# Kernel tuning notes

Measured on AMD Instinct MI355X. Metric: run time of the kernel, lower is better.

## Reference

```python
import jax, jax.numpy as jnp
import numpy as np

N = 50000      # nodes
E = 1_000_000  # edges (avg degree 20)
D = 64         # hidden dim
L = 3          # num dynamics layers
LN_EPS = 1e-5


def layernorm(h, g, b):
    mu = jnp.mean(h, axis=-1, keepdims=True)
    var = jnp.mean(jnp.square(h - mu), axis=-1, keepdims=True)
    return (h - mu) * jax.lax.rsqrt(var + LN_EPS) * g + b


def transformer_conv(h, src, dst, Wq, bq, Wk, bk, Wv, bv, Ws, bs):
    # PyG TransformerConv, heads=1, concat=False, beta=False, root_weight=True
    n = h.shape[0]
    d = Wq.shape[1]
    q = h @ Wq + bq            # [N, D] queries (dst side)
    k = h @ Wk + bk            # [N, D] keys   (src side)
    v = h @ Wv + bv            # [N, D] values (src side)
    logits = jnp.sum(q[dst] * k[src], axis=-1) / jnp.sqrt(jnp.asarray(d, h.dtype))  # [E]
    # segment softmax over incoming edges of each dst node
    m = jax.ops.segment_max(logits, dst, num_segments=n)      # [N]
    e = jnp.exp(logits - m[dst])                               # [E]
    s = jax.ops.segment_sum(e, dst, num_segments=n)            # [N]
    a = e / s[dst]                                             # [E]
    agg = jax.ops.segment_sum(a[:, None] * v[src], dst, num_segments=n)  # [N, D]
    return agg + h @ Ws + bs   # root/skip connection


def setup_inputs() -> dict:
    key = jax.random.key(0)
    ks = jax.random.split(key, 24)
    w = lambda k, shape: (jax.random.normal(k, shape, jnp.float32) * 0.05)
    inp = {
        "x": jax.random.normal(ks[0], (N, D), jnp.float32),
        "edge_index": jax.random.randint(ks[1], (2, E), 0, N, jnp.int32),
        # input_proj conv params
        "Wq0": w(ks[2], (D, D)), "bq0": w(ks[3], (D,)),
        "Wk0": w(ks[4], (D, D)), "bk0": w(ks[5], (D,)),
        "Wv0": w(ks[6], (D, D)), "bv0": w(ks[7], (D,)),
        "Ws0": w(ks[8], (D, D)), "bs0": w(ks[9], (D,)),
        "ln0_g": jnp.ones((D,), jnp.float32), "ln0_b": jnp.zeros((D,), jnp.float32),
        # stacked dynamics conv params [L, ...]
        "Wq": w(ks[10], (L, D, D)), "bq": w(ks[11], (L, D)),
        "Wk": w(ks[12], (L, D, D)), "bk": w(ks[13], (L, D)),
        "Wv": w(ks[14], (L, D, D)), "bv": w(ks[15], (L, D)),
        "Ws": w(ks[16], (L, D, D)), "bs": w(ks[17], (L, D)),
        "ln_g": jnp.ones((L, D), jnp.float32), "ln_b": jnp.zeros((L, D), jnp.float32),
    }
    return inp


def reference(x, edge_index, Wq0, bq0, Wk0, bk0, Wv0, bv0, Ws0, bs0, ln0_g, ln0_b,
              Wq, bq, Wk, bk, Wv, bv, Ws, bs, ln_g, ln_b):
    src, dst = edge_index[0], edge_index[1]
    h = transformer_conv(x, src, dst, Wq0, bq0, Wk0, bk0, Wv0, bv0, Ws0, bs0)
    h = jax.nn.relu(layernorm(h, ln0_g, ln0_b))
    # dropout is identity in eval mode
    for i in range(L):
        hi = transformer_conv(h, src, dst, Wq[i], bq[i], Wk[i], bk[i],
                              Wv[i], bv[i], Ws[i], bs[i])
        h = jax.nn.relu(layernorm(hi + h, ln_g[i], ln_b[i]))
    return h
```

## Files before the change

kernel.cpp:

```cpp
#include <hip/hip_runtime.h>
#include <math.h>


#define DD 64

typedef __attribute__((ext_vector_type(8))) _Float16 h8;
typedef __attribute__((ext_vector_type(2))) _Float16 h2;
typedef __attribute__((ext_vector_type(4))) float f32x4;

__device__ __forceinline__ unsigned short f2h(float f) {
    union { _Float16 h; unsigned short u; } c;
    c.h = (_Float16)f;
    return c.u;
}
__device__ __forceinline__ h2 u2h2(unsigned u) {
    union { unsigned u; h2 h; } c; c.u = u; return c.h;
}
__device__ __forceinline__ unsigned pk2u(float a, float b) {
    union { decltype(__builtin_amdgcn_cvt_pkrtz(0.f, 0.f)) h; unsigned u; } c;
    c.h = __builtin_amdgcn_cvt_pkrtz(a, b);
    return c.u;
}
__device__ __forceinline__ float h2dot(h2 a, h2 b, float c) {
#if __has_builtin(__builtin_amdgcn_fdot2)
    return __builtin_amdgcn_fdot2(a, b, c, false);
#else
    return fmaf((float)a[0], (float)b[0], fmaf((float)a[1], (float)b[1], c));
#endif
}

__global__ void count_rank(const int* __restrict__ dst, int* __restrict__ counts,
                           int* __restrict__ rank, int E) {
    int e = blockIdx.x * blockDim.x + threadIdx.x;
    if (e < E) rank[e] = atomicAdd(&counts[dst[e]], 1);
}

__global__ __launch_bounds__(1024) void scan_local(const int* __restrict__ counts,
                                                   int* __restrict__ localscan,
                                                   int* __restrict__ blockSums, int n) {
    __shared__ int sh[1024];
    int i = blockIdx.x * 1024 + threadIdx.x;
    int val = (i < n) ? counts[i] : 0;
    sh[threadIdx.x] = val;
    __syncthreads();
    for (int off = 1; off < 1024; off <<= 1) {
        int t = (threadIdx.x >= off) ? sh[threadIdx.x - off] : 0;
        __syncthreads();
        sh[threadIdx.x] += t;
        __syncthreads();
    }
    if (i < n) localscan[i] = sh[threadIdx.x] - val;
    if (threadIdx.x == 1023) blockSums[blockIdx.x] = sh[1023];
}

__global__ __launch_bounds__(64) void scan_tops(int* __restrict__ blockSums, int nb) {
    int i = threadIdx.x;
    int val = (i < nb) ? blockSums[i] : 0;
    int s = val;
#pragma unroll
    for (int off = 1; off < 64; off <<= 1) {
        int t = __shfl_up(s, off, 64);
        if (i >= off) s += t;
    }
    if (i < nb) blockSums[i] = s - val;
}

__global__ void emit_rowptr(const int* __restrict__ localscan,
                            const int* __restrict__ blockSums,
                            int* __restrict__ row_ptr, int n, int E) {
    int i = blockIdx.x * blockDim.x + threadIdx.x;
    if (i < n) row_ptr[i] = localscan[i] + blockSums[i >> 10];
    if (i == 0) row_ptr[n] = E;
}

__global__ void scatter_edges(const int* __restrict__ src, const int* __restrict__ dst,
                              const int* __restrict__ rank, const int* __restrict__ row_ptr,
                              int* __restrict__ col, int E) {
    int e = blockIdx.x * blockDim.x + threadIdx.x;
    if (e < E) col[row_ptr[dst[e]] + rank[e]] = src[e] << 8;
}

__global__ void prep_all(const float* __restrict__ x, unsigned short* __restrict__ hbf,
                         int nD,
                         const float* __restrict__ W0, const float* __restrict__ W1,
                         const float* __restrict__ W2, const float* __restrict__ W3,
                         const float* __restrict__ Wqs, const float* __restrict__ Wks,
                         const float* __restrict__ Wvs, const float* __restrict__ Wss,
                         unsigned short* __restrict__ Wt) {
    int i = blockIdx.x * blockDim.x + threadIdx.x;
    if (i < nD) { hbf[i] = f2h(x[i]); return; }
    int id = i - nD;
    if (id >= 16 * 4096) return;
    int mat = id >> 12, rem = id & 4095;
    int nn = rem >> 6, kk = rem & 63;
    int layer = mat >> 2, wh = mat & 3;
    const float* W;
    if (layer == 0) W = wh == 0 ? W0 : wh == 1 ? W1 : wh == 2 ? W2 : W3;
    else {
        const float* base = wh == 0 ? Wqs : wh == 1 ? Wks : wh == 2 ? Wvs : Wss;
        W = base + (size_t)(layer - 1) * 4096;
    }
    float val = W[kk * 64 + nn];
    if (wh == 0) val *= 0.125f;
    Wt[id] = f2h(val);
}

__global__ __launch_bounds__(256) void gemm_mfma(
    const unsigned short* __restrict__ hbf, const unsigned short* __restrict__ Wt,
    const float* __restrict__ Bq, const float* __restrict__ Bk,
    const float* __restrict__ Bv, const float* __restrict__ Bs,
    const float* __restrict__ hprev,
    unsigned short* __restrict__ qO, unsigned short* __restrict__ kvO,
    float* __restrict__ sO, int ntiles) {
    int lane = threadIdx.x & 63;
    int wave = threadIdx.x >> 6;
    int ml = lane & 15, ql = lane >> 4;

    const unsigned short* W = Wt + wave * 4096;
    h8 wfrag[4][2];
#pragma unroll
    for (int t = 0; t < 4; ++t)
#pragma unroll
        for (int kh = 0; kh < 2; ++kh)
            wfrag[t][kh] = *(const h8*)(W + (t * 16 + ml) * 64 + kh * 32 + ql * 8);

    const float* bias = wave == 0 ? Bq : wave == 1 ? Bk : wave == 2 ? Bv : Bs;
    float4 bias4[4];
#pragma unroll
    for (int t = 0; t < 4; ++t) {
        bias4[t] = *(const float4*)(bias + t * 16 + ql * 4);
        if (wave == 0) {
            bias4[t].x *= 0.125f; bias4[t].y *= 0.125f;
            bias4[t].z *= 0.125f; bias4[t].w *= 0.125f;
        }
    }

    for (int tile = blockIdx.x; tile < ntiles; tile += gridDim.x) {
        int node0 = tile * 16;
        h8 hfrag[2];
#pragma unroll
        for (int kh = 0; kh < 2; ++kh)
            hfrag[kh] = *(const h8*)(hbf + (size_t)(node0 + ml) * 64 + kh * 32 + ql * 8);
        f32x4 acc[4];
#pragma unroll
        for (int t = 0; t < 4; ++t) {
            acc[t][0] = bias4[t].x; acc[t][1] = bias4[t].y;
            acc[t][2] = bias4[t].z; acc[t][3] = bias4[t].w;
        }
#pragma unroll
        for (int t = 0; t < 4; ++t)
#pragma unroll
            for (int kh = 0; kh < 2; ++kh)
                acc[t] = __builtin_amdgcn_mfma_f32_16x16x32_f16(
                    wfrag[t][kh], hfrag[kh], acc[t], 0, 0, 0);

        size_t rowe = (size_t)(node0 + ml) * 64;
        if (wave == 0) {
#pragma unroll
            for (int t = 0; t < 4; ++t) {
                uint2 st;
                st.x = pk2u(acc[t][0], acc[t][1]);
                st.y = pk2u(acc[t][2], acc[t][3]);
                *(uint2*)(qO + rowe + t * 16 + ql * 4) = st;
            }
        } else if (wave == 3) {
#pragma unroll
            for (int t = 0; t < 4; ++t) {
                float4 st = {acc[t][0], acc[t][1], acc[t][2], acc[t][3]};
                if (hprev) {
                    float4 h4 = *(const float4*)(hprev + rowe + t * 16 + ql * 4);
                    st.x += h4.x; st.y += h4.y; st.z += h4.z; st.w += h4.w;
                }
                *(float4*)(sO + rowe + t * 16 + ql * 4) = st;
            }
        } else {
            size_t kve = (size_t)(node0 + ml) * 128 + (wave == 2 ? 64 : 0);
#pragma unroll
            for (int t = 0; t < 4; ++t) {
                uint2 st;
                st.x = pk2u(acc[t][0], acc[t][1]);
                st.y = pk2u(acc[t][2], acc[t][3]);
                *(uint2*)(kvO + kve + t * 16 + ql * 4) = st;
            }
        }
    }
}

__global__ __launch_bounds__(256) void attn_agg_ln(
    const unsigned short* __restrict__ qh, const unsigned short* __restrict__ kv,
    const float* __restrict__ sk,
    const int* __restrict__ row_ptr, const int* __restrict__ col,
    const float* __restrict__ g, const float* __restrict__ b,
    float* __restrict__ out, unsigned short* __restrict__ hbf_out, int n) {
    int node = blockIdx.x * 4 + (threadIdx.x >> 6);
    int lane = threadIdx.x & 63;
    if (node >= n) return;
    int grp = lane >> 3;
    int qi = lane & 7;

    size_t ro = (size_t)node * DD + qi * 8;
    uint4 qu = *(const uint4*)(qh + ro);
    float4 s4a = *(const float4*)(sk + ro);
    float4 s4b = *(const float4*)(sk + ro + 4);
    int beg = row_ptr[node], end = row_ptr[node + 1];

    float ssum = 0.0f;
    float4 aa = {0.f, 0.f, 0.f, 0.f}, ab = {0.f, 0.f, 0.f, 0.f};
    const char* kvb = (const char*)kv;

    int e = beg + grp;
    int cv = (e < end) ? col[e] : -1;
    for (int e0 = beg; e0 < end; e0 += 8) {
        bool act = cv >= 0;
        uint4 ku, vu;
        if (act) {
            const uint4* kp = (const uint4*)(kvb + cv) + qi;
            ku = kp[0];
            vu = kp[8];
        }
        e += 8;
        cv = (e < end) ? col[e] : -1;
        if (act) {
            float d = h2dot(u2h2(qu.x), u2h2(ku.x), 0.0f);
            d = h2dot(u2h2(qu.y), u2h2(ku.y), d);
            d = h2dot(u2h2(qu.z), u2h2(ku.z), d);
            d = h2dot(u2h2(qu.w), u2h2(ku.w), d);
            d += __shfl_xor(d, 1);
            d += __shfl_xor(d, 2);
            d += __shfl_xor(d, 4);
            float p = __expf(d);
            ssum += p;
            h2 v0 = u2h2(vu.x), v1 = u2h2(vu.y), v2 = u2h2(vu.z), v3 = u2h2(vu.w);
            aa.x = fmaf((float)v0[0], p, aa.x); aa.y = fmaf((float)v0[1], p, aa.y);
            aa.z = fmaf((float)v1[0], p, aa.z); aa.w = fmaf((float)v1[1], p, aa.w);
            ab.x = fmaf((float)v2[0], p, ab.x); ab.y = fmaf((float)v2[1], p, ab.y);
            ab.z = fmaf((float)v3[0], p, ab.z); ab.w = fmaf((float)v3[1], p, ab.w);
        }
    }

#pragma unroll
    for (int off = 8; off <= 32; off <<= 1) {
        ssum += __shfl_xor(ssum, off);
        aa.x += __shfl_xor(aa.x, off); aa.y += __shfl_xor(aa.y, off);
        aa.z += __shfl_xor(aa.z, off); aa.w += __shfl_xor(aa.w, off);
        ab.x += __shfl_xor(ab.x, off); ab.y += __shfl_xor(ab.y, off);
        ab.z += __shfl_xor(ab.z, off); ab.w += __shfl_xor(ab.w, off);
    }
    float inv = (end > beg) ? 1.0f / ssum : 0.0f;
    aa.x *= inv; aa.y *= inv; aa.z *= inv; aa.w *= inv;
    ab.x *= inv; ab.y *= inv; ab.z *= inv; ab.w *= inv;

    aa.x += s4a.x; aa.y += s4a.y; aa.z += s4a.z; aa.w += s4a.w;
    ab.x += s4b.x; ab.y += s4b.y; ab.z += s4b.z; ab.w += s4b.w;

    float s1 = aa.x + aa.y + aa.z + aa.w + ab.x + ab.y + ab.z + ab.w;
    s1 += __shfl_xor(s1, 1);
    s1 += __shfl_xor(s1, 2);
    s1 += __shfl_xor(s1, 4);
    float mu = s1 * (1.0f / DD);
    float dx0 = aa.x - mu, dx1 = aa.y - mu, dx2 = aa.z - mu, dx3 = aa.w - mu;
    float dx4 = ab.x - mu, dx5 = ab.y - mu, dx6 = ab.z - mu, dx7 = ab.w - mu;
    float s2v = dx0 * dx0 + dx1 * dx1 + dx2 * dx2 + dx3 * dx3
              + dx4 * dx4 + dx5 * dx5 + dx6 * dx6 + dx7 * dx7;
    s2v += __shfl_xor(s2v, 1);
    s2v += __shfl_xor(s2v, 2);
    s2v += __shfl_xor(s2v, 4);
    float var = s2v * (1.0f / DD);
    float is = rsqrtf(var + 1e-5f);
    float4 g4a = *(const float4*)(g + qi * 8);
    float4 g4b = *(const float4*)(g + qi * 8 + 4);
    float4 b4a = *(const float4*)(b + qi * 8);
    float4 b4b = *(const float4*)(b + qi * 8 + 4);
    float4 ya, yb;
    ya.x = fmaxf(dx0 * is * g4a.x + b4a.x, 0.0f);
    ya.y = fmaxf(dx1 * is * g4a.y + b4a.y, 0.0f);
    ya.z = fmaxf(dx2 * is * g4a.z + b4a.z, 0.0f);
    ya.w = fmaxf(dx3 * is * g4a.w + b4a.w, 0.0f);
    yb.x = fmaxf(dx4 * is * g4b.x + b4b.x, 0.0f);
    yb.y = fmaxf(dx5 * is * g4b.y + b4b.y, 0.0f);
    yb.z = fmaxf(dx6 * is * g4b.z + b4b.z, 0.0f);
    yb.w = fmaxf(dx7 * is * g4b.w + b4b.w, 0.0f);
    if (grp == 0) {
        *(float4*)(out + ro) = ya;
        *(float4*)(out + ro + 4) = yb;
        uint4 hv;
        hv.x = pk2u(ya.x, ya.y);
        hv.y = pk2u(ya.z, ya.w);
        hv.z = pk2u(yb.x, yb.y);
        hv.w = pk2u(yb.z, yb.w);
        *(uint4*)(hbf_out + ro) = hv;
    }
}

extern "C" void kernel_launch(void* const* d_in, const int* in_sizes, int n_in,
                              void* d_out, int out_size, void* d_ws, size_t ws_size,
                              hipStream_t stream) {
    const int D = DD;
    const float* x = (const float*)d_in[0];
    const int n = in_sizes[0] / D;
    const int* ei = (const int*)d_in[1];
    const int E = in_sizes[1] / 2;
    const int* srcp = ei;
    const int* dstp = ei + E;

    char* wsp = (char*)d_ws;
    auto take = [&](size_t bytes) {
        char* p = wsp;
        wsp += (bytes + 255) & ~(size_t)255;
        return (void*)p;
    };
    int* counts    = (int*)take((size_t)n * 4);
    int* row_ptr   = (int*)take((size_t)(n + 1) * 4);
    int* rank      = (int*)take((size_t)E * 4);
    int* col       = (int*)take((size_t)E * 4);
    int* localscan = (int*)take((size_t)n * 4);
    int* blockSums = (int*)take((size_t)1024 * 4);
    size_t fsz = (size_t)n * D * 4;
    unsigned short* qb  = (unsigned short*)take(fsz / 2);
    unsigned short* kvb = (unsigned short*)take(fsz);
    float* sb           = (float*)take(fsz);
    float* hA           = (float*)take(fsz);
    float* hB           = (float*)take(fsz);
    unsigned short* hbf = (unsigned short*)take(fsz / 2);
    unsigned short* Wt  = (unsigned short*)take((size_t)16 * 4096 * 2);

    hipMemsetAsync(counts, 0, (size_t)n * 4, stream);
    int tb = 256;
    int nbScan = (n + 1023) / 1024;
    count_rank<<<(E + tb - 1) / tb, tb, 0, stream>>>(dstp, counts, rank, E);
    scan_local<<<nbScan, 1024, 0, stream>>>(counts, localscan, blockSums, n);
    scan_tops<<<1, 64, 0, stream>>>(blockSums, nbScan);
    emit_rowptr<<<(n + tb - 1) / tb, tb, 0, stream>>>(localscan, blockSums, row_ptr, n, E);
    scatter_edges<<<(E + tb - 1) / tb, tb, 0, stream>>>(srcp, dstp, rank, row_ptr, col, E);

    int prep_total = n * D + 16 * 4096;
    prep_all<<<(prep_total + 255) / 256, 256, 0, stream>>>(
        x, hbf, n * D,
        (const float*)d_in[2], (const float*)d_in[4], (const float*)d_in[6],
        (const float*)d_in[8], (const float*)d_in[12], (const float*)d_in[14],
        (const float*)d_in[16], (const float*)d_in[18], Wt);

    const float* h = x;
    int ntiles = n / 16;
    int nba = (n + 3) / 4;
    for (int layer = 0; layer < 4; ++layer) {
        const float *bq_, *bk_, *bv_, *bs_, *g_, *b_;
        if (layer == 0) {
            bq_ = (const float*)d_in[3];  bk_ = (const float*)d_in[5];
            bv_ = (const float*)d_in[7];  bs_ = (const float*)d_in[9];
            g_  = (const float*)d_in[10]; b_  = (const float*)d_in[11];
        } else {
            int i = layer - 1;
            bq_ = (const float*)d_in[13] + (size_t)i * D;
            bk_ = (const float*)d_in[15] + (size_t)i * D;
            bv_ = (const float*)d_in[17] + (size_t)i * D;
            bs_ = (const float*)d_in[19] + (size_t)i * D;
            g_  = (const float*)d_in[20] + (size_t)i * D;
            b_  = (const float*)d_in[21] + (size_t)i * D;
        }
        gemm_mfma<<<512, 256, 0, stream>>>(hbf, Wt + (size_t)layer * 4 * 4096,
                                           bq_, bk_, bv_, bs_,
                                           layer == 0 ? nullptr : h,
                                           qb, kvb, sb, ntiles);
        float* hout = (layer == 3) ? (float*)d_out : ((layer & 1) ? hB : hA);
        attn_agg_ln<<<nba, 256, 0, stream>>>(qb, kvb, sb,
                                             row_ptr, col, g_, b_, hout, hbf, n);
        h = hout;
    }
}
```

Baseline: 393.9 us.

## Build CSR with per-block LDS histograms instead of global atomics

Replaces the global-atomic count/rank pass with a two-pass counting sort: each of 256 blocks builds a packed 16-bit-pair histogram of destination nodes in LDS, a column-wise prefix pass turns the block histograms into per-block offsets and totals, and a scatter pass recomputes local ranks with LDS atomics to place edges. This removes a million contended global atomics and the rank array. In exchange it uses about 100KB of LDS per block, which limits occupancy to one block per CU, and relies on per-block counts per node fitting in 16 bits. The prefix pass also reads the 256 block histograms serially for each node.

```diff
diff --git a/kernel.cpp b/kernel.cpp
--- a/kernel.cpp
+++ b/kernel.cpp
@@ -3,6 +3,7 @@
 
 
 #define DD 64
+#define NB_HIST 256
 
 typedef __attribute__((ext_vector_type(8))) _Float16 h8;
 typedef __attribute__((ext_vector_type(2))) _Float16 h2;
@@ -29,10 +30,39 @@
 #endif
 }
 
-__global__ void count_rank(const int* __restrict__ dst, int* __restrict__ counts,
-                           int* __restrict__ rank, int E) {
-    int e = blockIdx.x * blockDim.x + threadIdx.x;
-    if (e < E) rank[e] = atomicAdd(&counts[dst[e]], 1);
+__global__ __launch_bounds__(512) void hist_blk(const int* __restrict__ dst,
+                                                unsigned* __restrict__ cb,
+                                                int E, int nbw) {
+    extern __shared__ unsigned hist[];
+    int blk = blockIdx.x;
+    for (int w = threadIdx.x; w < nbw; w += blockDim.x) hist[w] = 0;
+    __syncthreads();
+    int chunk = (E + gridDim.x - 1) / gridDim.x;
+    int beg = blk * chunk;
+    int end = min(E, beg + chunk);
+    for (int e = beg + (int)threadIdx.x; e < end; e += blockDim.x) {
+        int d = dst[e];
+        atomicAdd(&hist[d >> 1], (d & 1) ? 0x10000u : 1u);
+    }
+    __syncthreads();
+    unsigned* out = cb + (size_t)blk * nbw;
+    for (int w = threadIdx.x; w < nbw; w += blockDim.x) out[w] = hist[w];
+}
+
+__global__ void prefix_blk(unsigned* __restrict__ cb, int* __restrict__ counts,
+                           int nbw, int nb, int n) {
+    int w = blockIdx.x * blockDim.x + threadIdx.x;
+    if (w >= nbw) return;
+    unsigned acc = 0;
+    for (int blk = 0; blk < nb; ++blk) {
+        size_t idx = (size_t)blk * nbw + w;
+        unsigned t = cb[idx];
+        cb[idx] = acc;
+        acc += t;
+    }
+    int b0 = 2 * w, b1 = 2 * w + 1;
+    counts[b0] = (int)(acc & 0xffffu);
+    if (b1 < n) counts[b1] = (int)(acc >> 16);
 }
 
 __global__ __launch_bounds__(1024) void scan_local(const int* __restrict__ counts,
@@ -73,11 +103,28 @@
     if (i == 0) row_ptr[n] = E;
 }
 
-__global__ void scatter_edges(const int* __restrict__ src, const int* __restrict__ dst,
-                              const int* __restrict__ rank, const int* __restrict__ row_ptr,
-                              int* __restrict__ col, int E) {
-    int e = blockIdx.x * blockDim.x + threadIdx.x;
-    if (e < E) col[row_ptr[dst[e]] + rank[e]] = src[e] << 8;
+__global__ __launch_bounds__(512) void scatter2(const int* __restrict__ src,
+                                                const int* __restrict__ dst,
+                                                const unsigned* __restrict__ cb,
+                                                const int* __restrict__ row_ptr,
+                                                int* __restrict__ col, int E, int nbw) {
+    extern __shared__ unsigned hist[];
+    int blk = blockIdx.x;
+    for (int w = threadIdx.x; w < nbw; w += blockDim.x) hist[w] = 0;
+    __syncthreads();
+    const unsigned* pref = cb + (size_t)blk * nbw;
+    int chunk = (E + gridDim.x - 1) / gridDim.x;
+    int beg = blk * chunk;
+    int end = min(E, beg + chunk);
+    for (int e = beg + (int)threadIdx.x; e < end; e += blockDim.x) {
+        int d = dst[e];
+        unsigned sh = (unsigned)(d & 1) * 16u;
+        unsigned old = atomicAdd(&hist[d >> 1], 1u << sh);
+        unsigned lr = (old >> sh) & 0xffffu;
+        unsigned pre = (pref[d >> 1] >> sh) & 0xffffu;
+        int slot = row_ptr[d] + (int)pre + (int)lr;
+        __builtin_nontemporal_store(src[e] << 8, &col[slot]);
+    }
 }
 
 __global__ void prep_all(const float* __restrict__ x, unsigned short* __restrict__ hbf,
@@ -302,6 +349,16 @@
     const int E = in_sizes[1] / 2;
     const int* srcp = ei;
     const int* dstp = ei + E;
+    const int nbw = (n + 1) / 2;
+
+    static bool s_attr = false;
+    if (!s_attr) {
+        s_attr = true;
+        (void)hipFuncSetAttribute((const void*)hist_blk,
+                                  hipFuncAttributeMaxDynamicSharedMemorySize, 102400);
+        (void)hipFuncSetAttribute((const void*)scatter2,
+                                  hipFuncAttributeMaxDynamicSharedMemorySize, 102400);
+    }
 
     char* wsp = (char*)d_ws;
     auto take = [&](size_t bytes) {
@@ -311,7 +368,7 @@
     };
     int* counts    = (int*)take((size_t)n * 4);
     int* row_ptr   = (int*)take((size_t)(n + 1) * 4);
-    int* rank      = (int*)take((size_t)E * 4);
+    unsigned* cb   = (unsigned*)take((size_t)NB_HIST * nbw * 4);
     int* col       = (int*)take((size_t)E * 4);
     int* localscan = (int*)take((size_t)n * 4);
     int* blockSums = (int*)take((size_t)1024 * 4);
@@ -324,14 +381,15 @@
     unsigned short* hbf = (unsigned short*)take(fsz / 2);
     unsigned short* Wt  = (unsigned short*)take((size_t)16 * 4096 * 2);
 
-    hipMemsetAsync(counts, 0, (size_t)n * 4, stream);
     int tb = 256;
+    size_t ldsH = (size_t)nbw * 4;
     int nbScan = (n + 1023) / 1024;
-    count_rank<<<(E + tb - 1) / tb, tb, 0, stream>>>(dstp, counts, rank, E);
+    hist_blk<<<NB_HIST, 512, ldsH, stream>>>(dstp, cb, E, nbw);
+    prefix_blk<<<(nbw + tb - 1) / tb, tb, 0, stream>>>(cb, counts, nbw, NB_HIST, n);
     scan_local<<<nbScan, 1024, 0, stream>>>(counts, localscan, blockSums, n);
     scan_tops<<<1, 64, 0, stream>>>(blockSums, nbScan);
     emit_rowptr<<<(n + tb - 1) / tb, tb, 0, stream>>>(localscan, blockSums, row_ptr, n, E);
-    scatter_edges<<<(E + tb - 1) / tb, tb, 0, stream>>>(srcp, dstp, rank, row_ptr, col, E);
+    scatter2<<<NB_HIST, 512, ldsH, stream>>>(srcp, dstp, cb, row_ptr, col, E, nbw);
 
     int prep_total = n * D + 16 * 4096;
     prep_all<<<(prep_total + 255) / 256, 256, 0, stream>>>(
```

New measurement: 432.8 us. +9.9%, slower.
